# Optimization experiments

Hardware: AMD Instinct MI355X
Metric: run time of the kernel (lower is better)

## Reference

```python
import jax, jax.numpy as jnp
import numpy as np

N = 50000
E = 800000
C = 128   # embed_channels
H = 4     # num_heads
D = C // H
POS = 3


def setup_inputs() -> dict:
    key = jax.random.key(0)
    ks = jax.random.split(key, 8)
    feat = jax.random.normal(ks[0], (N, C), dtype=jnp.float32)
    coord = jax.random.normal(ks[1], (N, POS), dtype=jnp.float32)
    graph = jax.random.randint(ks[2], (2, E), 0, N, dtype=jnp.int32)
    qkv_w = jax.random.normal(ks[3], (3 * C, C), dtype=jnp.float32) * (1.0 / np.sqrt(C))
    qkv_b = jax.random.normal(ks[4], (3 * C,), dtype=jnp.float32) * 0.02
    rpe_w = jax.random.normal(ks[5], (C, POS), dtype=jnp.float32) * (1.0 / np.sqrt(POS))
    rpe_b = jax.random.normal(ks[6], (C,), dtype=jnp.float32) * 0.02
    return {"feat": feat, "coord": coord, "graph": graph,
            "qkv_w": qkv_w, "qkv_b": qkv_b, "rpe_w": rpe_w, "rpe_b": rpe_b}


def _segment_softmax(x, seg, n):
    # x: [E, H], seg: [E] -> softmax over edges sharing the same destination node
    seg_max = jax.ops.segment_max(x, seg, num_segments=n)          # [N, H]
    seg_max = jnp.where(jnp.isfinite(seg_max), seg_max, 0.0)
    ex = jnp.exp(x - seg_max[seg])                                 # [E, H]
    seg_sum = jax.ops.segment_sum(ex, seg, num_segments=n)         # [N, H]
    return ex / seg_sum[seg]


def reference(feat, coord, graph, qkv_w, qkv_b, rpe_w, rpe_b):
    n = feat.shape[0]
    # qkv projection: [N, 3C] -> [N, 3, H, D]
    qkv = (feat @ qkv_w.T + qkv_b).reshape(n, 3, H, D)
    query, key, value = qkv[:, 0], qkv[:, 1], qkv[:, 2]            # each [N, H, D]
    dst, src = graph[0], graph[1]                                  # [E]
    # relative position encoding per edge
    rel = coord[dst] - coord[src]                                  # [E, 3]
    rpe = (rel @ rpe_w.T + rpe_b).reshape(-1, H, D)                # [E, H, D]
    # per-edge attention logits
    attn = (key[src] * query[dst] + rpe).sum(-1)                   # [E, H]
    attn = _segment_softmax(attn, dst, n)                          # [E, H]
    # weighted scatter-sum of values
    msg = attn[..., None] * value[src]                             # [E, H, D]
    out = jax.ops.segment_sum(msg, dst, num_segments=n)            # [N, H, D]
    return out.reshape(n, H * D)
```

## Files before the change

### kernel.cpp

```cpp
#include <hip/hip_runtime.h>
#include <hip/hip_bf16.h>

#define NN 50000
#define NE 800000
#define PAD 64
#define SCB 3125
#define CAB 196
#define CONVB 6298

typedef _Float16 fp16x8 __attribute__((ext_vector_type(8)));
typedef _Float16 half2 __attribute__((ext_vector_type(2)));
typedef __attribute__((ext_vector_type(8))) unsigned short ushort8;
typedef __attribute__((ext_vector_type(4))) float f32x4;

static __device__ __forceinline__ unsigned short f2h(float x) {
    _Float16 h = (_Float16)x;
    return __builtin_bit_cast(unsigned short, h);
}
static __device__ __forceinline__ float dot2(half2 a, half2 b, float c) {
#if __has_builtin(__builtin_amdgcn_fdot2)
    return __builtin_amdgcn_fdot2(a, b, c, false);
#else
    return c + (float)a.x * (float)b.x + (float)a.y * (float)b.y;
#endif
}

__global__ __launch_bounds__(256) void k_pre(
    const float* __restrict__ feat, const float* __restrict__ w,
    unsigned short* __restrict__ feat16, unsigned short* __restrict__ w16,
    const float* __restrict__ coord, const float* __restrict__ rpe_w,
    const float* __restrict__ rpe_b, float* __restrict__ ca,
    float* __restrict__ cb,
    const int* __restrict__ graph, int* __restrict__ cnt,
    unsigned short* __restrict__ sorted_src)
{
    const int b = blockIdx.x;
    const int t = threadIdx.x;
    if (b < SCB) {
        int e = b * 256 + t;
        int dst = graph[e];
        int src = graph[NE + e];
        int slot = atomicAdd(&cnt[dst], 1);
        if (slot < PAD) sorted_src[(dst << 6) + slot] = (unsigned short)src;
        return;
    }
    if (b < SCB + CAB) {
        __shared__ float s_rw[12];
        __shared__ float s_rb[4];
        if (t < 12) {
            int h = t / 3, p = t % 3;
            float s = 0.f;
            for (int d = 0; d < 32; ++d) s += rpe_w[(h * 32 + d) * 3 + p];
            s_rw[t] = s;
        } else if (t < 16) {
            int h = t - 12;
            float s = 0.f;
            for (int d = 0; d < 32; ++d) s += rpe_b[h * 32 + d];
            s_rb[h] = s;
        }
        __syncthreads();
        int n = (b - SCB) * 256 + t;
        if (n < NN) {
            float c0 = coord[n * 3 + 0], c1 = coord[n * 3 + 1], c2 = coord[n * 3 + 2];
#pragma unroll
            for (int h = 0; h < 4; ++h) {
                float a = c0 * s_rw[h * 3 + 0] + c1 * s_rw[h * 3 + 1] + c2 * s_rw[h * 3 + 2];
                ca[n * 4 + h] = a;
                cb[n * 4 + h] = a + s_rb[h];
            }
        }
        return;
    }
    const int totalA = NN * 128 / 4;
    int idx = (b - SCB - CAB) * 256 + t;
    if (idx < totalA) {
        float4 a = ((const float4*)feat)[idx];
        ((ushort4*)feat16)[idx] = make_ushort4(f2h(a.x), f2h(a.y), f2h(a.z), f2h(a.w));
    } else {
        int k = idx - totalA;
        float4 a = ((const float4*)w)[k];
        ((ushort4*)w16)[k] = make_ushort4(f2h(a.x), f2h(a.y), f2h(a.z), f2h(a.w));
    }
}

__global__ __launch_bounds__(256) void qkv_gemm(
    const unsigned short* __restrict__ feat16, const unsigned short* __restrict__ w16,
    const float* __restrict__ bias, unsigned short* __restrict__ qbuf16,
    unsigned short* __restrict__ kvbuf)
{
    __shared__ __align__(16) unsigned short Ah[128][40];
    __shared__ __align__(16) unsigned short Bh[128][40];

    const int t    = threadIdx.x;
    const int bi   = blockIdx.x / 3;
    const int role = blockIdx.x - bi * 3;
    const int bm = bi * 128;
    const int bc = role * 128;

    const int wave = t >> 6;
    const int lane = t & 63;
    const int wr = wave & 1;
    const int wc = wave >> 1;
    const int qd = lane >> 4;
    const int l15 = lane & 15;

    f32x4 acc[4][4];
#pragma unroll
    for (int i = 0; i < 4; ++i)
#pragma unroll
        for (int j = 0; j < 4; ++j)
            acc[i][j] = (f32x4){0.f, 0.f, 0.f, 0.f};

    for (int ks = 0; ks < 4; ++ks) {
        const int k0 = ks * 32;
        if (ks) __syncthreads();
#pragma unroll
        for (int c = 0; c < 2; ++c) {
            int idx = c * 256 + t;
            int r  = idx >> 2;
            int c8 = (idx & 3) * 8;
            int ga = bm + r;
            ushort8 a8 = (ga < NN)
                ? *(const ushort8*)(feat16 + (size_t)ga * 128 + k0 + c8)
                : (ushort8){0,0,0,0,0,0,0,0};
            *(ushort8*)&Ah[r][c8] = a8;
            *(ushort8*)&Bh[r][c8] = *(const ushort8*)(w16 + (size_t)(bc + r) * 128 + k0 + c8);
        }
        __syncthreads();
        fp16x8 af[4];
#pragma unroll
        for (int i = 0; i < 4; ++i)
            af[i] = *(const fp16x8*)&Ah[wr * 64 + 16 * i + l15][qd * 8];
#pragma unroll
        for (int j = 0; j < 4; ++j) {
            fp16x8 bf = *(const fp16x8*)&Bh[wc * 64 + 16 * j + l15][qd * 8];
#pragma unroll
            for (int i = 0; i < 4; ++i)
                acc[i][j] = __builtin_amdgcn_mfma_f32_16x16x32_f16(af[i], bf, acc[i][j], 0, 0, 0);
        }
    }

    float bj[4];
#pragma unroll
    for (int j = 0; j < 4; ++j)
        bj[j] = bias[bc + wc * 64 + 16 * j + l15];

    unsigned short* Ct = &Ah[0][0];
    const int isQ = (role == 0);
    const int half = (role == 1) ? 0 : 128;
    const int relRowW = wr * 16 + qd * 4;

    for (int i = 0; i < 4; ++i) {
        __syncthreads();
#pragma unroll
        for (int j = 0; j < 4; ++j) {
            int col = wc * 64 + 16 * j + l15;
#pragma unroll
            for (int rg = 0; rg < 4; ++rg)
                Ct[(relRowW + rg) * 136 + col] = f2h(acc[i][j][rg] + bj[j]);
        }
        __syncthreads();
#pragma unroll
        for (int p = 0; p < 2; ++p) {
            int linear = p * 256 + t;
            int rr = linear >> 4;
            int cc = linear & 15;
            int absRow = bm + 16 * i + rr + ((rr >> 4) * 48);
            if (absRow < NN) {
                ushort8 val = *(const ushort8*)&Ct[rr * 136 + cc * 8];
                if (isQ) *(ushort8*)(qbuf16 + (size_t)absRow * 128 + cc * 8) = val;
                else     *(ushort8*)(kvbuf + (size_t)absRow * 256 + half + cc * 8) = val;
            }
        }
    }
}

__global__ __launch_bounds__(256) void node_attn(
    const unsigned short* __restrict__ qbuf16, const unsigned short* __restrict__ kvbuf,
    const float* __restrict__ ca, const float* __restrict__ cb,
    const int* __restrict__ cnt, const unsigned short* __restrict__ sorted_src,
    float* __restrict__ out)
{
    const int t = threadIdx.x;
    const int n = blockIdx.x * 8 + (t >> 5);
    if (n >= NN) return;
    const int j = t & 31;
    const int h = j >> 3;
    const int j8 = j * 8;
    const int h4 = h * 4;

    const uint2 qv = *(const uint2*)((const char*)qbuf16 + (size_t)n * 256 + j8);
    const half2 qh01 = __builtin_bit_cast(half2, qv.x);
    const half2 qh23 = __builtin_bit_cast(half2, qv.y);
    const float cbh = cb[n * 4 + h];
    const int start = n << 6;
    int d = cnt[n];
    if (d > PAD) d = PAD;

    float4 acc = make_float4(0.f, 0.f, 0.f, 0.f);
    float den = 0.f;
    const char* kvp = (const char*)kvbuf;
    const char* cap = (const char*)ca;

    int i = 0;
    for (; i + 3 < d; i += 4) {
        ushort4 s4 = *(const ushort4*)(sorted_src + start + i);
        unsigned o0 = (unsigned)s4.x << 9;
        unsigned o1 = (unsigned)s4.y << 9;
        unsigned o2 = (unsigned)s4.z << 9;
        unsigned o3 = (unsigned)s4.w << 9;
        uint2 k0 = *(const uint2*)(kvp + o0 + j8);
        uint2 k1 = *(const uint2*)(kvp + o1 + j8);
        uint2 k2 = *(const uint2*)(kvp + o2 + j8);
        uint2 k3 = *(const uint2*)(kvp + o3 + j8);
        uint2 v0 = *(const uint2*)(kvp + o0 + 256 + j8);
        uint2 v1 = *(const uint2*)(kvp + o1 + 256 + j8);
        uint2 v2 = *(const uint2*)(kvp + o2 + 256 + j8);
        uint2 v3 = *(const uint2*)(kvp + o3 + 256 + j8);
        float a0 = *(const float*)(cap + (o0 >> 5) + h4);
        float a1 = *(const float*)(cap + (o1 >> 5) + h4);
        float a2 = *(const float*)(cap + (o2 >> 5) + h4);
        float a3 = *(const float*)(cap + (o3 >> 5) + h4);

        float p0 = dot2(qh01, __builtin_bit_cast(half2, k0.x),
                   dot2(qh23, __builtin_bit_cast(half2, k0.y), 0.f));
        float p1 = dot2(qh01, __builtin_bit_cast(half2, k1.x),
                   dot2(qh23, __builtin_bit_cast(half2, k1.y), 0.f));
        float p2 = dot2(qh01, __builtin_bit_cast(half2, k2.x),
                   dot2(qh23, __builtin_bit_cast(half2, k2.y), 0.f));
        float p3 = dot2(qh01, __builtin_bit_cast(half2, k3.x),
                   dot2(qh23, __builtin_bit_cast(half2, k3.y), 0.f));
        p0 += __shfl_xor(p0, 1); p1 += __shfl_xor(p1, 1);
        p2 += __shfl_xor(p2, 1); p3 += __shfl_xor(p3, 1);
        p0 += __shfl_xor(p0, 2); p1 += __shfl_xor(p1, 2);
        p2 += __shfl_xor(p2, 2); p3 += __shfl_xor(p3, 2);
        p0 += __shfl_xor(p0, 4); p1 += __shfl_xor(p1, 4);
        p2 += __shfl_xor(p2, 4); p3 += __shfl_xor(p3, 4);

        float e0 = __expf(p0 + cbh - a0);
        float e1 = __expf(p1 + cbh - a1);
        float e2 = __expf(p2 + cbh - a2);
        float e3 = __expf(p3 + cbh - a3);
        den += (e0 + e1) + (e2 + e3);
        half2 v0a = __builtin_bit_cast(half2, v0.x), v0b = __builtin_bit_cast(half2, v0.y);
        half2 v1a = __builtin_bit_cast(half2, v1.x), v1b = __builtin_bit_cast(half2, v1.y);
        half2 v2a = __builtin_bit_cast(half2, v2.x), v2b = __builtin_bit_cast(half2, v2.y);
        half2 v3a = __builtin_bit_cast(half2, v3.x), v3b = __builtin_bit_cast(half2, v3.y);
        acc.x += e0 * (float)v0a.x + e1 * (float)v1a.x + e2 * (float)v2a.x + e3 * (float)v3a.x;
        acc.y += e0 * (float)v0a.y + e1 * (float)v1a.y + e2 * (float)v2a.y + e3 * (float)v3a.y;
        acc.z += e0 * (float)v0b.x + e1 * (float)v1b.x + e2 * (float)v2b.x + e3 * (float)v3b.x;
        acc.w += e0 * (float)v0b.y + e1 * (float)v1b.y + e2 * (float)v2b.y + e3 * (float)v3b.y;
    }
    for (; i < d; ++i) {
        unsigned o0 = (unsigned)sorted_src[start + i] << 9;
        uint2 k0 = *(const uint2*)(kvp + o0 + j8);
        uint2 v0 = *(const uint2*)(kvp + o0 + 256 + j8);
        float a0 = *(const float*)(cap + (o0 >> 5) + h4);
        float p0 = dot2(qh01, __builtin_bit_cast(half2, k0.x),
                   dot2(qh23, __builtin_bit_cast(half2, k0.y), 0.f));
        p0 += __shfl_xor(p0, 1);
        p0 += __shfl_xor(p0, 2);
        p0 += __shfl_xor(p0, 4);
        float e = __expf(p0 + cbh - a0);
        den += e;
        half2 va = __builtin_bit_cast(half2, v0.x);
        half2 vb = __builtin_bit_cast(half2, v0.y);
        acc.x += e * (float)va.x;
        acc.y += e * (float)va.y;
        acc.z += e * (float)vb.x;
        acc.w += e * (float)vb.y;
    }

    float inv = (den > 0.f) ? 1.0f / den : 0.f;
    float4 o = make_float4(acc.x * inv, acc.y * inv, acc.z * inv, acc.w * inv);
    ((float4*)(out + (size_t)n * 128))[j] = o;
}

extern "C" void kernel_launch(void* const* d_in, const int* in_sizes, int n_in,
                              void* d_out, int out_size, void* d_ws, size_t ws_size,
                              hipStream_t stream) {
    const float* feat  = (const float*)d_in[0];
    const float* coord = (const float*)d_in[1];
    const int*   graph = (const int*)d_in[2];
    const float* qkv_w = (const float*)d_in[3];
    const float* qkv_b = (const float*)d_in[4];
    const float* rpe_w = (const float*)d_in[5];
    const float* rpe_b = (const float*)d_in[6];
    float* out = (float*)d_out;

    unsigned short* qbuf16 = (unsigned short*)d_ws;
    unsigned short* kvbuf  = qbuf16 + (size_t)NN * 128;
    unsigned short* feat16 = kvbuf + (size_t)NN * 256;
    unsigned short* w16    = feat16 + (size_t)NN * 128;
    int*            cnt    = (int*)(w16 + 384 * 128);
    unsigned short* sorted_src = (unsigned short*)(cnt + NN);
    float* ca = (float*)(sorted_src + (size_t)NN * PAD);
    float* cb = ca + (size_t)NN * 4;

    hipMemsetAsync(cnt, 0, NN * sizeof(int), stream);

    k_pre    <<<dim3(SCB + CAB + CONVB), 256, 0, stream>>>(feat, qkv_w, feat16, w16,
                                                           coord, rpe_w, rpe_b, ca, cb,
                                                           graph, cnt, sorted_src);
    qkv_gemm <<<dim3(391 * 3), 256, 0, stream>>>(feat16, w16, qkv_b, qbuf16, kvbuf);
    node_attn<<<dim3((NN + 7) / 8), 256, 0, stream>>>(qbuf16, kvbuf, ca, cb,
                                                      cnt, sorted_src, out);
}
```

Baseline: 214.5 us.

## Fuse preprocessing into QKV GEMM with in-kernel fp32-to-fp16 conversion

Removes the separate pre-kernel. The GEMM now loads fp32 feat and weights directly and converts them to fp16 while staging into shared memory, so the fp16 copies no longer have to be written and read back. A fourth block role per row tile takes over the edge-bucketing atomics, with 8 edges per thread, plus the coordinate-projection work, so these overlap with the GEMM blocks. In exchange, weights are converted redundantly in every block, global load traffic per tile doubles, and the atomic blocks run alongside the GEMM blocks.

```diff
diff --git a/kernel.cpp b/kernel.cpp
--- a/kernel.cpp
+++ b/kernel.cpp
@@ -4,9 +4,7 @@
 #define NN 50000
 #define NE 800000
 #define PAD 64
-#define SCB 3125
 #define CAB 196
-#define CONVB 6298
 
 typedef _Float16 fp16x8 __attribute__((ext_vector_type(8)));
 typedef _Float16 half2 __attribute__((ext_vector_type(2)));
@@ -25,75 +23,70 @@
 #endif
 }
 
-__global__ __launch_bounds__(256) void k_pre(
+__global__ __launch_bounds__(256) void qkv_gemm(
     const float* __restrict__ feat, const float* __restrict__ w,
-    unsigned short* __restrict__ feat16, unsigned short* __restrict__ w16,
+    const float* __restrict__ bias, unsigned short* __restrict__ qbuf16,
+    unsigned short* __restrict__ kvbuf,
     const float* __restrict__ coord, const float* __restrict__ rpe_w,
     const float* __restrict__ rpe_b, float* __restrict__ ca,
     float* __restrict__ cb,
     const int* __restrict__ graph, int* __restrict__ cnt,
     unsigned short* __restrict__ sorted_src)
 {
-    const int b = blockIdx.x;
-    const int t = threadIdx.x;
-    if (b < SCB) {
-        int e = b * 256 + t;
-        int dst = graph[e];
-        int src = graph[NE + e];
-        int slot = atomicAdd(&cnt[dst], 1);
-        if (slot < PAD) sorted_src[(dst << 6) + slot] = (unsigned short)src;
+    const int t    = threadIdx.x;
+    const int role = blockIdx.x & 3;
+    const int bi   = blockIdx.x >> 2;
+
+    if (role == 3) {
+        if (bi < CAB) {
+            __shared__ float s_rw[12];
+            __shared__ float s_rb[4];
+            if (t < 12) {
+                int h = t / 3, p = t % 3;
+                float s = 0.f;
+                for (int d = 0; d < 32; ++d) s += rpe_w[(h * 32 + d) * 3 + p];
+                s_rw[t] = s;
+            } else if (t < 16) {
+                int h = t - 12;
+                float s = 0.f;
+                for (int d = 0; d < 32; ++d) s += rpe_b[h * 32 + d];
+                s_rb[h] = s;
+            }
+            __syncthreads();
+            int n = bi * 256 + t;
+            if (n < NN) {
+                float c0 = coord[n * 3 + 0], c1 = coord[n * 3 + 1], c2 = coord[n * 3 + 2];
+#pragma unroll
+                for (int h = 0; h < 4; ++h) {
+                    float a = c0 * s_rw[h * 3 + 0] + c1 * s_rw[h * 3 + 1] + c2 * s_rw[h * 3 + 2];
+                    ca[n * 4 + h] = a;
+                    cb[n * 4 + h] = a + s_rb[h];
+                }
+            }
+        }
+        const int e0 = bi * 256 + t;
+        const int stride = 391 * 256;
+        int dsts[8], srcs[8], slots[8];
+        bool ok[8];
+#pragma unroll
+        for (int u = 0; u < 8; ++u) {
+            int e = e0 + u * stride;
+            ok[u] = (e < NE);
+            if (ok[u]) { dsts[u] = graph[e]; srcs[u] = graph[NE + e]; }
+        }
+#pragma unroll
+        for (int u = 0; u < 8; ++u)
+            if (ok[u]) slots[u] = atomicAdd(&cnt[dsts[u]], 1);
+#pragma unroll
+        for (int u = 0; u < 8; ++u)
+            if (ok[u] && slots[u] < PAD)
+                sorted_src[(dsts[u] << 6) + slots[u]] = (unsigned short)srcs[u];
         return;
     }
-    if (b < SCB + CAB) {
-        __shared__ float s_rw[12];
-        __shared__ float s_rb[4];
-        if (t < 12) {
-            int h = t / 3, p = t % 3;
-            float s = 0.f;
-            for (int d = 0; d < 32; ++d) s += rpe_w[(h * 32 + d) * 3 + p];
-            s_rw[t] = s;
-        } else if (t < 16) {
-            int h = t - 12;
-            float s = 0.f;
-            for (int d = 0; d < 32; ++d) s += rpe_b[h * 32 + d];
-            s_rb[h] = s;
-        }
-        __syncthreads();
-        int n = (b - SCB) * 256 + t;
-        if (n < NN) {
-            float c0 = coord[n * 3 + 0], c1 = coord[n * 3 + 1], c2 = coord[n * 3 + 2];
-#pragma unroll
-            for (int h = 0; h < 4; ++h) {
-                float a = c0 * s_rw[h * 3 + 0] + c1 * s_rw[h * 3 + 1] + c2 * s_rw[h * 3 + 2];
-                ca[n * 4 + h] = a;
-                cb[n * 4 + h] = a + s_rb[h];
-            }
-        }
-        return;
-    }
-    const int totalA = NN * 128 / 4;
-    int idx = (b - SCB - CAB) * 256 + t;
-    if (idx < totalA) {
-        float4 a = ((const float4*)feat)[idx];
-        ((ushort4*)feat16)[idx] = make_ushort4(f2h(a.x), f2h(a.y), f2h(a.z), f2h(a.w));
-    } else {
-        int k = idx - totalA;
-        float4 a = ((const float4*)w)[k];
-        ((ushort4*)w16)[k] = make_ushort4(f2h(a.x), f2h(a.y), f2h(a.z), f2h(a.w));
-    }
-}
-
-__global__ __launch_bounds__(256) void qkv_gemm(
-    const unsigned short* __restrict__ feat16, const unsigned short* __restrict__ w16,
-    const float* __restrict__ bias, unsigned short* __restrict__ qbuf16,
-    unsigned short* __restrict__ kvbuf)
-{
+
     __shared__ __align__(16) unsigned short Ah[128][40];
     __shared__ __align__(16) unsigned short Bh[128][40];
 
-    const int t    = threadIdx.x;
-    const int bi   = blockIdx.x / 3;
-    const int role = blockIdx.x - bi * 3;
     const int bm = bi * 128;
     const int bc = role * 128;
 
@@ -120,11 +113,20 @@
             int r  = idx >> 2;
             int c8 = (idx & 3) * 8;
             int ga = bm + r;
-            ushort8 a8 = (ga < NN)
-                ? *(const ushort8*)(feat16 + (size_t)ga * 128 + k0 + c8)
-                : (ushort8){0,0,0,0,0,0,0,0};
+            ushort8 a8 = (ushort8){0,0,0,0,0,0,0,0};
+            if (ga < NN) {
+                const float* ap = feat + (size_t)ga * 128 + k0 + c8;
+                float4 x = *(const float4*)ap;
+                float4 y = *(const float4*)(ap + 4);
+                a8 = (ushort8){f2h(x.x), f2h(x.y), f2h(x.z), f2h(x.w),
+                               f2h(y.x), f2h(y.y), f2h(y.z), f2h(y.w)};
+            }
             *(ushort8*)&Ah[r][c8] = a8;
-            *(ushort8*)&Bh[r][c8] = *(const ushort8*)(w16 + (size_t)(bc + r) * 128 + k0 + c8);
+            const float* bp = w + (size_t)(bc + r) * 128 + k0 + c8;
+            float4 bx = *(const float4*)bp;
+            float4 by = *(const float4*)(bp + 4);
+            *(ushort8*)&Bh[r][c8] = (ushort8){f2h(bx.x), f2h(bx.y), f2h(bx.z), f2h(bx.w),
+                                              f2h(by.x), f2h(by.y), f2h(by.z), f2h(by.w)};
         }
         __syncthreads();
         fp16x8 af[4];
@@ -290,19 +292,16 @@
 
     unsigned short* qbuf16 = (unsigned short*)d_ws;
     unsigned short* kvbuf  = qbuf16 + (size_t)NN * 128;
-    unsigned short* feat16 = kvbuf + (size_t)NN * 256;
-    unsigned short* w16    = feat16 + (size_t)NN * 128;
-    int*            cnt    = (int*)(w16 + 384 * 128);
+    int*            cnt    = (int*)(kvbuf + (size_t)NN * 256);
     unsigned short* sorted_src = (unsigned short*)(cnt + NN);
     float* ca = (float*)(sorted_src + (size_t)NN * PAD);
     float* cb = ca + (size_t)NN * 4;
 
     hipMemsetAsync(cnt, 0, NN * sizeof(int), stream);
 
-    k_pre    <<<dim3(SCB + CAB + CONVB), 256, 0, stream>>>(feat, qkv_w, feat16, w16,
-                                                           coord, rpe_w, rpe_b, ca, cb,
-                                                           graph, cnt, sorted_src);
-    qkv_gemm <<<dim3(391 * 3), 256, 0, stream>>>(feat16, w16, qkv_b, qbuf16, kvbuf);
+    qkv_gemm <<<dim3(391 * 4), 256, 0, stream>>>(feat, qkv_w, qkv_b, qbuf16, kvbuf,
+                                                 coord, rpe_w, rpe_b, ca, cb,
+                                                 graph, cnt, sorted_src);
     node_attn<<<dim3((NN + 7) / 8), 256, 0, stream>>>(qbuf16, kvbuf, ca, cb,
                                                       cnt, sorted_src, out);
 }
```

Result: faster. 204.0 us (-4.9%).
